# Kernel tuning notes

Hardware: AMD Instinct MI355X
Metric: run time of the kernel (lower is better)

The kernel has to match this reference:

```python
import jax, jax.numpy as jnp
import numpy as np

ANCHORS = np.array([[4.63,1.97,1.74],[6.93,2.51,2.84],[6.37,2.85,3.19],[10.5,2.94,3.47],
                    [12.29,2.9,3.87],[0.5,2.53,0.98],[2.11,0.77,1.47],[1.7,0.6,1.28],
                    [0.73,0.67,1.77],[0.41,0.41,1.07]], dtype=np.float32)  # [10,3] nuScenes anchor sizes
BINS = 20          # anchor_size_bins
TEXT_DIM = 3 * BINS
NUM_PROPOSALS = 200
NMS_K = 3


def _vector_values():
    la = np.log(ANCHORS)
    return np.linspace(la.min() - 0.1, la.max() - 0.1, BINS).astype(np.float32)


def _anchor_vecs_normed():
    # soft_relu_bin_vectors: soft-bin log-anchors into BINS bins per dim, dim-major flatten
    vals = _vector_values()
    inc = vals[1] - vals[0]
    la = np.log(ANCHORS)                                      # [10,3]
    v = np.clip((la[:, :, None] - vals[None, None, :]) / inc, 0.0, 1.0)  # [10,3,BINS]
    v = v.reshape(10, TEXT_DIM)
    return (v / (1e-8 + np.linalg.norm(v, axis=1, keepdims=True))).astype(np.float32)


def conv2d(x, w, b=None):
    y = jax.lax.conv_general_dilated(x, w, (1, 1), 'SAME',
                                     dimension_numbers=('NCHW', 'OIHW', 'NCHW'))
    if b is not None:
        y = y + b[None, :, None, None]
    return y


def iou_sim_vec(a):
    # vectorized form of the triple-nested loop: prod over dims of min/max ratio
    mn = jnp.minimum(a[:, None, :], a[None, :, :])
    mx = jnp.maximum(a[:, None, :], a[None, :, :])
    return jnp.prod(mn / mx, axis=-1)                         # [10,10]


def setup_inputs() -> dict:
    key = jax.random.key(0)
    ks = jax.random.split(key, 8)
    B, Cin, hid, H, W = 2, 512, 128, 180, 180
    feats = jax.random.normal(ks[0], (B, Cin, H, W), jnp.float32)
    w_shared = jax.random.normal(ks[1], (hid, Cin, 3, 3), jnp.float32) * 0.02
    b_shared = jnp.zeros((hid,), jnp.float32)
    w_bb = jax.random.normal(ks[2], (hid, hid, 3, 3), jnp.float32) * 0.05
    gamma_bb = jnp.ones((hid,), jnp.float32)
    beta_bb = jnp.zeros((hid,), jnp.float32)
    w_hm = jax.random.normal(ks[3], (TEXT_DIM, hid, 3, 3), jnp.float32) * 0.05
    b_hm = jnp.zeros((TEXT_DIM,), jnp.float32)
    thr_scale = jnp.ones((1,), jnp.float32)                   # Threshold2d scale
    logit_scale = jnp.ones((1,), jnp.float32) * np.log(1.0 / 0.07)
    logit_bias = jnp.ones((1,), jnp.float32) * (-10.0)
    w_enc = jax.random.normal(ks[4], (hid, 3), jnp.float32) * 0.1  # Conv1d(3->hid, k=1)
    anchor_vecs = jnp.asarray(_anchor_vecs_normed())
    xs = jnp.arange(W, dtype=jnp.float32) + 0.5
    ys = jnp.arange(H, dtype=jnp.float32) + 0.5
    gy, gx = jnp.meshgrid(ys, xs, indexing='ij')
    bev_pos = jnp.stack([gx.reshape(-1), gy.reshape(-1)], axis=-1)  # [H*W, 2]
    return dict(feats=feats, w_shared=w_shared, b_shared=b_shared, w_bb=w_bb,
                gamma_bb=gamma_bb, beta_bb=beta_bb, w_hm=w_hm, b_hm=b_hm,
                thr_scale=thr_scale, logit_scale=logit_scale, logit_bias=logit_bias,
                w_enc=w_enc, anchor_vecs=anchor_vecs, bev_pos=bev_pos)


def reference(feats, w_shared, b_shared, w_bb, gamma_bb, beta_bb, w_hm, b_hm,
              thr_scale, logit_scale, logit_bias, w_enc, anchor_vecs, bev_pos):
    B, _, H, W = feats.shape
    # shared conv
    lidar_feat = conv2d(feats, w_shared, b_shared)            # [B,hid,H,W]
    # BasicBlock2D: conv + (inference) BN + ReLU
    x = conv2d(lidar_feat, w_bb)
    x = jax.nn.relu(x * gamma_bb[None, :, None, None] + beta_bb[None, :, None, None])
    # heatmap conv -> Threshold2d (sigmoid((x - thresholds) * scale))
    vec = conv2d(x, w_hm, b_hm)                               # [B,60,H,W]
    thresholds = jnp.asarray(np.tile(_vector_values(), 3))[None, :, None, None]
    vec = jax.nn.sigmoid((vec - thresholds) * thr_scale[0])
    # cosine sim vs normalized anchor bin-vectors -> per-class heatmap
    vecn = vec / (1e-8 + jnp.linalg.norm(vec, axis=1, keepdims=True))
    sim = jnp.einsum('bchw,kc->bkhw', vecn, anchor_vecs)      # [B,10,H,W]
    heatmap = jax.nn.sigmoid(logit_scale[0] * sim + logit_bias[0])
    # NMS: keep only local maxima within nms_kernel_size window
    local_max = jax.lax.reduce_window(heatmap, -jnp.inf, jax.lax.max,
                                      (1, 1, NMS_K, NMS_K), (1, 1, 1, 1), 'SAME')
    hm_nms = jnp.where(heatmap == local_max, heatmap, 0.0)
    # top-k proposals over classes x positions
    flat = hm_nms.reshape(B, -1)                              # [B, 10*H*W]
    top_scores, top_idx = jax.lax.top_k(flat, NUM_PROPOSALS)
    top_labels = top_idx // (H * W)                           # [B,P]
    top_pos = top_idx % (H * W)                               # [B,P]
    # gather proposal features, heatmap scores and bev positions
    hid = lidar_feat.shape[1]
    lidar_flat = lidar_feat.reshape(B, hid, H * W)
    idx_f = jnp.broadcast_to(top_pos[:, None, :], (B, hid, NUM_PROPOSALS))
    query_feat = jnp.take_along_axis(lidar_flat, idx_f, axis=2)  # [B,hid,P]
    hm_flat = heatmap.reshape(B, 10, H * W)
    idx_h = jnp.broadcast_to(top_pos[:, None, :], (B, 10, NUM_PROPOSALS))
    query_hm_score = jnp.take_along_axis(hm_flat, idx_h, axis=2)  # [B,10,P]
    query_pos = bev_pos[top_pos]                              # [B,P,2]
    # anchor value encoding (Conv1d(3->hid,k=1) on log-anchor sizes of top classes)
    top_anchor = jnp.log(jnp.asarray(ANCHORS))[top_labels]    # [B,P,3]
    query_feat = query_feat + jnp.einsum('cd,bpd->bcp', w_enc, top_anchor)
    sims = iou_sim_vec(jnp.asarray(ANCHORS))                  # [10,10] anchor IoU similarity
    return heatmap, top_scores, top_labels, query_feat, query_pos, query_hm_score, sims
```

## Files before the change

### kernel.cpp

```cpp
#include <hip/hip_runtime.h>
#include <math.h>


#define HW 180
#define NPIX 32400
#define NCLS 10
#define NPROP 200
#define HID 128
#define TDIM 60
#define NBIG (NCLS*NPIX)

#define TH_LO  (-0.9915981193)
#define TH_STEP (0.1789675812)

__constant__ float c_anchors[10][3] = {
  {4.63f,1.97f,1.74f},{6.93f,2.51f,2.84f},{6.37f,2.85f,3.19f},{10.5f,2.94f,3.47f},
  {12.29f,2.9f,3.87f},{0.5f,2.53f,0.98f},{2.11f,0.77f,1.47f},{1.7f,0.6f,1.28f},
  {0.73f,0.67f,1.77f},{0.41f,0.41f,1.07f}};

using f16x8 = _Float16 __attribute__((ext_vector_type(8)));
using f16x4 = _Float16 __attribute__((ext_vector_type(4)));
using f32x4 = float    __attribute__((ext_vector_type(4)));

#define GLD_LDS16(g, l) __builtin_amdgcn_global_load_lds( \
    (__attribute__((address_space(1))) void*)(g), \
    (__attribute__((address_space(3))) void*)(l), 16, 0, 0)

template<int CIN, int KS, int HALVES>
__global__ void transpose_w_mfma(const float* __restrict__ w, _Float16* __restrict__ dst,
                                 int cout) {
  const int N = HALVES * KS * 36864;
  int i = blockIdx.x * 256 + threadIdx.x;
  if (i >= N) return;
  int j = i & 7;
  int lane = (i >> 3) & 63;
  int mf = (i >> 9) & 3;
  int rest = i >> 11;
  int tsl = rest % 9; rest /= 9;
  int t = (tsl % 3) * 3 + (tsl / 3);
  int plane = rest & 1; rest >>= 1;
  int ks = rest % KS; int h = rest / KS;
  int co = h * 64 + mf * 16 + (lane & 15);
  int ch = ks * 32 + (lane >> 4) * 8 + j;
  float v = (co < cout) ? w[((size_t)co * CIN + ch) * 9 + t] : 0.f;
  _Float16 hi = (_Float16)v;
  dst[i] = plane ? (_Float16)(v - (float)hi) : hi;
}

__global__ __launch_bounds__(256)
void convert_feats(const float* __restrict__ feats, _Float16* __restrict__ X1) {
  int px = blockIdx.x * 256 + threadIdx.x;
  int b = blockIdx.y >> 4, ks = blockIdx.y & 15;
  if (px >= NPIX) return;
  const float* src = feats + ((size_t)(b * 512 + ks * 32)) * NPIX + px;
  float v[32];
#pragma unroll
  for (int c = 0; c < 32; ++c) v[c] = src[(size_t)c * NPIX];
  f16x8 hv[4], lv[4];
#pragma unroll
  for (int c = 0; c < 32; ++c) {
    _Float16 h = (_Float16)v[c];
    hv[c >> 3][c & 7] = h;
    lv[c >> 3][c & 7] = (_Float16)(v[c] - (float)h);
  }
  size_t ob = ((size_t)(b * 16 + ks) * NPIX + px) * 32;
#pragma unroll
  for (int i = 0; i < 4; ++i) {
    *(f16x8*)(X1 + ob + i * 8) = hv[i];
    *(f16x8*)(X1 + 33177600u + ob + i * 8) = lv[i];
  }
}

template<int KS, int EPI>
__global__ __launch_bounds__(256, 2)
void conv_mfma(const _Float16* __restrict__ X, const _Float16* __restrict__ W,
               const float* __restrict__ p0, const float* __restrict__ p1,
               float* __restrict__ out0, _Float16* __restrict__ outX,
               const float* __restrict__ thr_scale, const float* __restrict__ logit_scale,
               const float* __restrict__ logit_bias, const float* __restrict__ anchor_vecs) {
  constexpr unsigned XPS = 2u * KS * NPIX * 32;
  extern __shared__ _Float16 dlds[];
  _Float16* lds_x = dlds;
  _Float16* lds_w = dlds + 25344;
  float* lds_av = (float*)(dlds + 37632);

  const int x0 = blockIdx.x * 16;
  const int y0 = blockIdx.y * 20;
  const int b  = (EPI == 2) ? blockIdx.z : (blockIdx.z >> 1);
  const int h  = (EPI == 2) ? 0 : (blockIdx.z & 1);
  const int tid = threadIdx.x;
  const int wave = tid >> 6;
  const int lane = tid & 63;
  const int xl = lane & 15, kg = lane >> 4;

  {
    unsigned* p = (unsigned*)lds_x;
    for (int i = tid; i < 12672; i += 256) p[i] = 0u;
    if (EPI == 2)
      for (int i = tid; i < 600; i += 256) lds_av[i] = anchor_vecs[i];
  }

  unsigned offs[13]; unsigned okb = 0;
#pragma unroll
  for (int s = 0; s < 13; ++s) {
    int inst = wave + 4 * s;
    int c = inst * 64 + lane;
    bool valid = (inst < 50) && (c < 3168);
    int plane = (c >= 1584) ? 1 : 0;
    int cc = c - plane * 1584;
    int px = cc >> 2, q = cc & 3;
    int r = px / 18, xx = px - r * 18;
    int gy = y0 - 1 + r, gx = x0 - 1 + xx;
    bool ok = valid && ((unsigned)gy < 180u) && ((unsigned)gx < 180u);
    offs[s] = ok ? ((unsigned)((b * KS) * NPIX + gy * 180 + gx) * 32u + (unsigned)q * 8u
                    + (unsigned)plane * XPS) : 0u;
    okb |= (ok ? 1u : 0u) << s;
  }

  f32x4 acc[4][5];
#pragma unroll
  for (int mf = 0; mf < 4; ++mf)
#pragma unroll
    for (int f = 0; f < 5; ++f) acc[mf][f] = (f32x4){0.f, 0.f, 0.f, 0.f};

  const _Float16* gwb = W + (size_t)(h * KS) * 36864;
  for (int ks = 0; ks < KS; ++ks) {
    const unsigned kof = (unsigned)ks * (NPIX * 32u);
    const _Float16* gw = gwb + (size_t)ks * 36864;
#pragma unroll
    for (int g = 0; g < 3; ++g) {
      __syncthreads();
      if (g == 0) {
#pragma unroll
        for (int s = 0; s < 13; ++s) {
          if (okb & (1u << s))
            GLD_LDS16(X + (size_t)(offs[s] + kof), lds_x + (wave + 4 * s) * 512);
        }
      }
#pragma unroll
      for (int s = 0; s < 6; ++s) {
        int c2 = wave + 4 * s;
        int pl = c2 / 12, idx = c2 - pl * 12;
        GLD_LDS16(gw + pl * 18432 + g * 6144 + idx * 512 + lane * 8,
                  lds_w + pl * 6144 + idx * 512);
      }
      __syncthreads();

      f16x8 bfh[7], bfl[7];
#pragma unroll
      for (int rr = 0; rr < 7; ++rr) {
        int lo = ((5 * wave + rr) * 18 + xl + g) * 32 + kg * 8;
        bfh[rr] = *(const f16x8*)(lds_x + lo);
        bfl[rr] = *(const f16x8*)(lds_x + 12672 + lo);
      }
#pragma unroll
      for (int ky = 0; ky < 3; ++ky) {
        const _Float16* wt = lds_w + ky * 2048 + lane * 8;
        f16x8 ah[4], al[4];
#pragma unroll
        for (int mf = 0; mf < 4; ++mf) {
          ah[mf] = *(const f16x8*)(wt + mf * 512);
          al[mf] = *(const f16x8*)(wt + 6144 + mf * 512);
        }
#pragma unroll
        for (int mf = 0; mf < 4; ++mf)
#pragma unroll
          for (int f = 0; f < 5; ++f) {
            acc[mf][f] = __builtin_amdgcn_mfma_f32_16x16x32_f16(ah[mf], bfh[f + ky], acc[mf][f], 0, 0, 0);
            acc[mf][f] = __builtin_amdgcn_mfma_f32_16x16x32_f16(ah[mf], bfl[f + ky], acc[mf][f], 0, 0, 0);
            acc[mf][f] = __builtin_amdgcn_mfma_f32_16x16x32_f16(al[mf], bfh[f + ky], acc[mf][f], 0, 0, 0);
          }
      }
    }
  }

  const int x = x0 + xl;
  if (EPI != 2) {
    if (x >= HW) return;
#pragma unroll
    for (int mf = 0; mf < 4; ++mf) {
      const int cobase = h * 64 + mf * 16 + kg * 4;
      f32x4 q0 = *(const f32x4*)(p0 + cobase);
      f32x4 q1 = (EPI == 1) ? *(const f32x4*)(p1 + cobase) : (f32x4){0.f,0.f,0.f,0.f};
#pragma unroll
      for (int f = 0; f < 5; ++f) {
        const int y = y0 + 5 * wave + f;
        const int kso = cobase >> 5, c32 = cobase & 31;
        size_t nidx = ((size_t)(b * 4 + kso) * NPIX + (size_t)y * 180 + x) * 32 + c32;
        if (EPI == 0) {
          f32x4 v;
          f16x4 h4, l4;
#pragma unroll
          for (int r = 0; r < 4; ++r) {
            float z = acc[mf][f][r] + q0[r];
            v[r] = z;
            _Float16 hh = (_Float16)z;
            h4[r] = hh;
            l4[r] = (_Float16)(z - (float)hh);
          }
          *(f32x4*)(out0 + nidx) = v;
          *(f16x4*)(outX + nidx) = h4;
          *(f16x4*)(outX + 8294400u + nidx) = l4;
        } else {
          f16x4 h4, l4;
#pragma unroll
          for (int r = 0; r < 4; ++r) {
            float z = fmaf(acc[mf][f][r], q0[r], q1[r]);
            z = fmaxf(z, 0.f);
            _Float16 hh = (_Float16)z;
            h4[r] = hh;
            l4[r] = (_Float16)(z - (float)hh);
          }
          *(f16x4*)(outX + nidx) = h4;
          *(f16x4*)(outX + 8294400u + nidx) = l4;
        }
      }
    }
  } else {
    const float s  = thr_scale[0];
    const float ls = logit_scale[0];
    const float lb = logit_bias[0];
    float bh4[4][4], th4[4][4];
    bool vmask[4];
#pragma unroll
    for (int mf = 0; mf < 4; ++mf) {
      const int cb = mf * 16 + kg * 4;
      vmask[mf] = (cb < TDIM);
#pragma unroll
      for (int r = 0; r < 4; ++r) {
        bh4[mf][r] = vmask[mf] ? p0[cb + r] : 0.f;
        th4[mf][r] = (float)(TH_LO + (double)((cb + r) % 20) * TH_STEP);
      }
    }
#pragma unroll
    for (int f = 0; f < 5; ++f) {
      const int y = y0 + 5 * wave + f;
      float v[4][4];
      float s2 = 0.f;
#pragma unroll
      for (int mf = 0; mf < 4; ++mf)
#pragma unroll
        for (int r = 0; r < 4; ++r) {
          float z = acc[mf][f][r] + bh4[mf][r];
          float t = (z - th4[mf][r]) * s;
          float vv = vmask[mf] ? 1.f / (1.f + expf(-t)) : 0.f;
          v[mf][r] = vv;
          s2 = fmaf(vv, vv, s2);
        }
      s2 += __shfl_xor(s2, 16);
      s2 += __shfl_xor(s2, 32);
      const float rs = 1.f / (1e-8f + sqrtf(s2));
      float hm[10];
#pragma unroll
      for (int k = 0; k < 10; ++k) {
        float d = 0.f;
#pragma unroll
        for (int mf = 0; mf < 4; ++mf) {
          const int cb = mf * 16 + kg * 4;
          f32x4 a = vmask[mf] ? *(const f32x4*)(lds_av + k * TDIM + cb)
                              : (f32x4){0.f, 0.f, 0.f, 0.f};
#pragma unroll
          for (int r = 0; r < 4; ++r) d = fmaf(v[mf][r], a[r], d);
        }
        d += __shfl_xor(d, 16);
        d += __shfl_xor(d, 32);
        hm[k] = 1.f / (1.f + expf(-fmaf(ls, d * rs, lb)));
      }
      if (y < HW && x < HW) {
#pragma unroll
        for (int j = 0; j < 3; ++j) {
          int k = kg + 4 * j;
          if (k < NCLS)
            out0[((size_t)(b * NCLS + k) * HW + y) * HW + x] = hm[k];
        }
      }
    }
  }
}

__global__ void sims_kernel(float* __restrict__ out_sims) {
  int t = threadIdx.x;
  if (t < 100) {
    int i = t / 10, j = t % 10;
    float r = 1.f;
#pragma unroll
    for (int d = 0; d < 3; ++d) {
      float ai = c_anchors[i][d], aj = c_anchors[j][d];
      r *= fminf(ai, aj) / fmaxf(ai, aj);
    }
    out_sims[t] = r;
  }
}

__global__ __launch_bounds__(256)
void nms_kernel(const float* __restrict__ hm, float* __restrict__ ckey,
                int* __restrict__ cidx, int* __restrict__ cnt) {
  __shared__ int lcnt[2];
  __shared__ int lbase[2];
  const int tid = threadIdx.x;
  if (tid < 2) lcnt[tid] = 0;
  __syncthreads();

  int i = blockIdx.x * 256 + tid;
  bool surv = false; float v = 0.f; int bk = 0, p = 0;
  if (i < 2 * NBIG) {
    int x = i % HW; int y = (i / HW) % HW; int plane = i / NPIX;
    v = hm[i];
    float m = v;
#pragma unroll
    for (int dy = -1; dy <= 1; ++dy)
#pragma unroll
      for (int dx = -1; dx <= 1; ++dx) {
        int yy = y + dy, xx = x + dx;
        if ((unsigned)yy < (unsigned)HW && (unsigned)xx < (unsigned)HW)
          m = fmaxf(m, hm[((size_t)plane * NPIX) + yy * HW + xx]);
      }
    if (v == m) {
      surv = true;
      bk = i / NBIG;
      p = atomicAdd(&lcnt[bk], 1);
    }
  }
  __syncthreads();
  if (tid < 2 && lcnt[tid] > 0)
    lbase[tid] = atomicAdd(&cnt[tid], lcnt[tid]);
  __syncthreads();
  if (surv) {
    int slot = lbase[bk] + p;
    ckey[(size_t)bk * NBIG + slot] = v;
    cidx[(size_t)bk * NBIG + slot] = i - bk * NBIG;
  }
}

__global__ __launch_bounds__(1024)
void topk_kernel(const float* __restrict__ ckey, const int* __restrict__ cidx,
                 const int* __restrict__ cnt, const float* __restrict__ heatmap,
                 const float* __restrict__ bev_pos, float* __restrict__ out,
                 int* __restrict__ iws) {
  const int b = blockIdx.x;
  const int tid = threadIdx.x;
  const float* keys = ckey + (size_t)b * NBIG;
  const int* idxs = cidx + (size_t)b * NBIG;

  __shared__ unsigned hist[256];
  __shared__ unsigned sh_prefix;
  __shared__ int sh_want, sh_n;
  __shared__ int cntGT, cntTie;
  __shared__ unsigned gt_key[256], gt_idx[256];
  __shared__ unsigned tie_idx[2048];

  if (tid == 0) sh_n = cnt[b];
  __syncthreads();
  const int n = sh_n;

  unsigned prefix = 0; int want = NPROP;
  for (int shift = 24; shift >= 0; shift -= 8) {
    if (tid < 256) hist[tid] = 0u;
    __syncthreads();
    for (int i = tid; i < n; i += 1024) {
      unsigned k = __float_as_uint(keys[i]);
      bool match = (shift == 24) || ((k >> (shift + 8)) == (prefix >> (shift + 8)));
      if (match) atomicAdd(&hist[(k >> shift) & 255], 1u);
    }
    __syncthreads();
    if (tid == 0) {
      int cum = 0; int bsel = 0; sh_want = want;
      for (int bin = 255; bin >= 0; --bin) {
        cum += (int)hist[bin];
        if (cum >= want) { bsel = bin; sh_want = want - (cum - (int)hist[bin]); break; }
      }
      sh_prefix = prefix | ((unsigned)bsel << shift);
      cntGT = 0; cntTie = 0;
    }
    __syncthreads();
    prefix = sh_prefix; want = sh_want;
    __syncthreads();
  }
  const unsigned T = prefix;

  for (int i = tid; i < n; i += 1024) {
    unsigned k = __float_as_uint(keys[i]);
    if (k > T) {
      int p = atomicAdd(&cntGT, 1);
      if (p < 256) { gt_key[p] = k; gt_idx[p] = (unsigned)idxs[i]; }
    } else if (k == T) {
      int p = atomicAdd(&cntTie, 1);
      if (p < 2048) tie_idx[p] = (unsigned)idxs[i];
    }
  }
  __syncthreads();
  const int nGT = min(cntGT, 256);
  const int nTie = min(cntTie, 2048);

  for (int i = tid; i < 256; i += 1024)
    if (i >= nGT) { gt_key[i] = 0u; gt_idx[i] = 0xFFFFFFFFu; }
  for (int i = tid; i < 2048; i += 1024)
    if (i >= nTie) tie_idx[i] = 0xFFFFFFFFu;
  __syncthreads();

  for (int k2 = 2; k2 <= 256; k2 <<= 1) {
    for (int j = k2 >> 1; j > 0; j >>= 1) {
      for (int i = tid; i < 256; i += 1024) {
        int ixj = i ^ j;
        if (ixj > i) {
          unsigned ka = gt_key[i], kb = gt_key[ixj];
          unsigned ia = gt_idx[i], ib = gt_idx[ixj];
          bool firstA = (ka > kb) || (ka == kb && ia < ib);
          bool up = ((i & k2) == 0);
          if (up ? !firstA : firstA) {
            gt_key[i] = kb; gt_key[ixj] = ka;
            gt_idx[i] = ib; gt_idx[ixj] = ia;
          }
        }
      }
      __syncthreads();
    }
  }
  for (int k2 = 2; k2 <= 2048; k2 <<= 1) {
    for (int j = k2 >> 1; j > 0; j >>= 1) {
      for (int i = tid; i < 2048; i += 1024) {
        int ixj = i ^ j;
        if (ixj > i) {
          unsigned ia = tie_idx[i], ib = tie_idx[ixj];
          bool firstA = ia < ib;
          bool up = ((i & k2) == 0);
          if (up ? !firstA : firstA) { tie_idx[i] = ib; tie_idx[ixj] = ia; }
        }
      }
      __syncthreads();
    }
  }

  for (int r = tid; r < NPROP; r += 1024) {
    unsigned idx; float score;
    if (r < nGT) { idx = gt_idx[r]; score = __uint_as_float(gt_key[r]); }
    else         { idx = tie_idx[r - nGT]; score = __uint_as_float(T); }
    int label = (int)(idx / NPIX);
    int pos = (int)(idx - (unsigned)label * NPIX);
    out[648000 + b * NPROP + r] = score;
    out[648400 + b * NPROP + r] = (float)label;
    out[700000 + (b * NPROP + r) * 2 + 0] = bev_pos[pos * 2 + 0];
    out[700000 + (b * NPROP + r) * 2 + 1] = bev_pos[pos * 2 + 1];
#pragma unroll
    for (int k = 0; k < NCLS; ++k)
      out[700800 + (b * NCLS + k) * NPROP + r] = heatmap[(size_t)(b * NCLS + k) * NPIX + pos];
    iws[b * NPROP + r] = pos;
    iws[2 * NPROP + b * NPROP + r] = label;
  }
}

__global__ void gather_qf_kernel(const float* __restrict__ lidar, const float* __restrict__ w_enc,
                                 const int* __restrict__ iws, float* __restrict__ out_qf) {
  int p = blockIdx.x % NPROP;
  int b = blockIdx.x / NPROP;
  int c = threadIdx.x;
  int pos = iws[b * NPROP + p];
  int label = iws[2 * NPROP + b * NPROP + p];
  float la0 = logf(c_anchors[label][0]);
  float la1 = logf(c_anchors[label][1]);
  float la2 = logf(c_anchors[label][2]);
  float dot = w_enc[c * 3 + 0] * la0 + w_enc[c * 3 + 1] * la1 + w_enc[c * 3 + 2] * la2;
  float g = lidar[((size_t)(b * 4 + (c >> 5)) * NPIX + pos) * 32 + (c & 31)];
  out_qf[((size_t)b * HID + c) * NPROP + p] = g + dot;
}

extern "C" void kernel_launch(void* const* d_in, const int* in_sizes, int n_in,
                              void* d_out, int out_size, void* d_ws, size_t ws_size,
                              hipStream_t stream) {
  (void)in_sizes; (void)n_in; (void)out_size; (void)ws_size;
  const float* feats       = (const float*)d_in[0];
  const float* w_shared    = (const float*)d_in[1];
  const float* b_shared    = (const float*)d_in[2];
  const float* w_bb        = (const float*)d_in[3];
  const float* gamma_bb    = (const float*)d_in[4];
  const float* beta_bb     = (const float*)d_in[5];
  const float* w_hm        = (const float*)d_in[6];
  const float* b_hm        = (const float*)d_in[7];
  const float* thr_scale   = (const float*)d_in[8];
  const float* logit_scale = (const float*)d_in[9];
  const float* logit_bias  = (const float*)d_in[10];
  const float* w_enc       = (const float*)d_in[11];
  const float* anchor_vecs = (const float*)d_in[12];
  const float* bev_pos     = (const float*)d_in[13];
  float* out = (float*)d_out;

  float* ws = (float*)d_ws;
  size_t off = 0;
  _Float16* X1 = (_Float16*)(ws + off); off += 33177600;
  _Float16* X2 = (_Float16*)(ws + off); off += 8294400;
  float* lidarN = ws + off; off += 8294400;
  _Float16* X3 = (_Float16*)(ws + off); off += 8294400;
  _Float16* W1 = (_Float16*)(ws + off); off += 589824;
  _Float16* W2 = (_Float16*)(ws + off); off += 147456;
  _Float16* W3 = (_Float16*)(ws + off); off += 73728;
  float* ckey  = ws + off; off += (size_t)2 * NBIG;
  int*   cidx  = (int*)(ws + off); off += (size_t)2 * NBIG;
  int*   iws   = (int*)(ws + off); off += 800;
  int*   cnt   = (int*)(ws + off);

  transpose_w_mfma<512,16,2><<<(2*16*36864 + 255)/256, 256, 0, stream>>>(w_shared, W1, 128);
  transpose_w_mfma<128, 4,2><<<(2*4*36864  + 255)/256, 256, 0, stream>>>(w_bb, W2, 128);
  transpose_w_mfma<128, 4,1><<<(1*4*36864  + 255)/256, 256, 0, stream>>>(w_hm, W3, 60);
  convert_feats<<<dim3(127, 32), 256, 0, stream>>>(feats, X1);

  const unsigned CONV_LDS = (25344 + 12288) * sizeof(_Float16);
  const unsigned HEAD_LDS = CONV_LDS + 600 * sizeof(float);
  dim3 cgrid(12, 9, 4);
  conv_mfma<16,0><<<cgrid, 256, CONV_LDS, stream>>>(X1, W1, b_shared, nullptr, lidarN, X2,
                                                    nullptr, nullptr, nullptr, nullptr);
  conv_mfma<4, 1><<<cgrid, 256, CONV_LDS, stream>>>(X2, W2, gamma_bb, beta_bb, nullptr, X3,
                                                    nullptr, nullptr, nullptr, nullptr);
  dim3 hgrid(12, 9, 2);
  conv_mfma<4, 2><<<hgrid, 256, HEAD_LDS, stream>>>(X3, W3, b_hm, nullptr, out, nullptr,
                                                    thr_scale, logit_scale, logit_bias,
                                                    anchor_vecs);

  sims_kernel<<<1, 128, 0, stream>>>(out + 704800);
  hipMemsetAsync(cnt, 0, 2 * sizeof(int), stream);
  nms_kernel<<<(2*NBIG + 255)/256, 256, 0, stream>>>(out, ckey, cidx, cnt);
  topk_kernel<<<2, 1024, 0, stream>>>(ckey, cidx, cnt, out, bev_pos, out, iws);
  gather_qf_kernel<<<2*NPROP, 128, 0, stream>>>(lidarN, w_enc, iws, out + 648800);
}
```

Baseline: 539.0 us.

## Shrink conv row tile, double-buffer weight loads, and merge prep kernels

Each conv block now covers 12 rows instead of 20, which gives a 12x15 grid and smaller LDS and accumulator footprints. The two non-head convs keep two LDS weight buffers so the next weight slice is loaded while the current one is computed. The weight transposes, feature conversion, anchor-similarity computation and counter reset are merged into one prep kernel to cut launch overhead. In exchange the halo overhead per output row rises and LDS per block goes up for the double-buffered variants, which may limit occupancy.

```diff
diff --git a/kernel.cpp b/kernel.cpp
--- a/kernel.cpp
+++ b/kernel.cpp
@@ -26,11 +26,9 @@
     (__attribute__((address_space(1))) void*)(g), \
     (__attribute__((address_space(3))) void*)(l), 16, 0, 0)
 
-template<int CIN, int KS, int HALVES>
-__global__ void transpose_w_mfma(const float* __restrict__ w, _Float16* __restrict__ dst,
-                                 int cout) {
-  const int N = HALVES * KS * 36864;
-  int i = blockIdx.x * 256 + threadIdx.x;
+__device__ __forceinline__ void w_tr(const float* __restrict__ w, _Float16* __restrict__ dst,
+                                     int CIN, int KS, int HALVES, int cout, int i) {
+  int N = HALVES * KS * 36864;
   if (i >= N) return;
   int j = i & 7;
   int lane = (i >> 3) & 63;
@@ -48,27 +46,53 @@
 }
 
 __global__ __launch_bounds__(256)
-void convert_feats(const float* __restrict__ feats, _Float16* __restrict__ X1) {
-  int px = blockIdx.x * 256 + threadIdx.x;
-  int b = blockIdx.y >> 4, ks = blockIdx.y & 15;
-  if (px >= NPIX) return;
-  const float* src = feats + ((size_t)(b * 512 + ks * 32)) * NPIX + px;
-  float v[32];
-#pragma unroll
-  for (int c = 0; c < 32; ++c) v[c] = src[(size_t)c * NPIX];
-  f16x8 hv[4], lv[4];
-#pragma unroll
-  for (int c = 0; c < 32; ++c) {
-    _Float16 h = (_Float16)v[c];
-    hv[c >> 3][c & 7] = h;
-    lv[c >> 3][c & 7] = (_Float16)(v[c] - (float)h);
-  }
-  size_t ob = ((size_t)(b * 16 + ks) * NPIX + px) * 32;
-#pragma unroll
-  for (int i = 0; i < 4; ++i) {
-    *(f16x8*)(X1 + ob + i * 8) = hv[i];
-    *(f16x8*)(X1 + 33177600u + ob + i * 8) = lv[i];
-  }
+void prep_kernel(const float* __restrict__ w_shared, const float* __restrict__ w_bb,
+                 const float* __restrict__ w_hm, const float* __restrict__ feats,
+                 _Float16* __restrict__ W1, _Float16* __restrict__ W2,
+                 _Float16* __restrict__ W3, _Float16* __restrict__ X1,
+                 float* __restrict__ out_sims, int* __restrict__ cnt) {
+  int bid = blockIdx.x;
+  const int tid = threadIdx.x;
+  if (bid < 4608) { w_tr(w_shared, W1, 512, 16, 2, 128, bid * 256 + tid); return; }
+  bid -= 4608;
+  if (bid < 1152) { w_tr(w_bb, W2, 128, 4, 2, 128, bid * 256 + tid); return; }
+  bid -= 1152;
+  if (bid < 576)  { w_tr(w_hm, W3, 128, 4, 1, 60, bid * 256 + tid); return; }
+  bid -= 576;
+  if (bid < 4064) {
+    int px = (bid % 127) * 256 + tid;
+    int bks = bid / 127; int b = bks >> 4; int ks = bks & 15;
+    if (px >= NPIX) return;
+    const float* src = feats + ((size_t)(b * 512 + ks * 32)) * NPIX + px;
+    float v[32];
+#pragma unroll
+    for (int c = 0; c < 32; ++c) v[c] = src[(size_t)c * NPIX];
+    f16x8 hv[4], lv[4];
+#pragma unroll
+    for (int c = 0; c < 32; ++c) {
+      _Float16 h = (_Float16)v[c];
+      hv[c >> 3][c & 7] = h;
+      lv[c >> 3][c & 7] = (_Float16)(v[c] - (float)h);
+    }
+    size_t ob = ((size_t)(b * 16 + ks) * NPIX + px) * 32;
+#pragma unroll
+    for (int i = 0; i < 4; ++i) {
+      *(f16x8*)(X1 + ob + i * 8) = hv[i];
+      *(f16x8*)(X1 + 33177600u + ob + i * 8) = lv[i];
+    }
+    return;
+  }
+  if (tid < 100) {
+    int i = tid / 10, j = tid % 10;
+    float r = 1.f;
+#pragma unroll
+    for (int d = 0; d < 3; ++d) {
+      float ai = c_anchors[i][d], aj = c_anchors[j][d];
+      r *= fminf(ai, aj) / fmaxf(ai, aj);
+    }
+    out_sims[tid] = r;
+  }
+  if (tid == 128) { cnt[0] = 0; cnt[1] = 0; }
 }
 
 template<int KS, int EPI>
@@ -79,13 +103,15 @@
                const float* __restrict__ thr_scale, const float* __restrict__ logit_scale,
                const float* __restrict__ logit_bias, const float* __restrict__ anchor_vecs) {
   constexpr unsigned XPS = 2u * KS * NPIX * 32;
+  constexpr bool DBUF = (EPI != 2);
   extern __shared__ _Float16 dlds[];
   _Float16* lds_x = dlds;
-  _Float16* lds_w = dlds + 25344;
-  float* lds_av = (float*)(dlds + 37632);
+  _Float16* wA = dlds + 16128;
+  _Float16* wB = dlds + 28416;
+  float* lds_av = (float*)(dlds + 28416);
 
   const int x0 = blockIdx.x * 16;
-  const int y0 = blockIdx.y * 20;
+  const int y0 = blockIdx.y * 12;
   const int b  = (EPI == 2) ? blockIdx.z : (blockIdx.z >> 1);
   const int h  = (EPI == 2) ? 0 : (blockIdx.z & 1);
   const int tid = threadIdx.x;
@@ -95,19 +121,19 @@
 
   {
     unsigned* p = (unsigned*)lds_x;
-    for (int i = tid; i < 12672; i += 256) p[i] = 0u;
+    for (int i = tid; i < 8064; i += 256) p[i] = 0u;
     if (EPI == 2)
       for (int i = tid; i < 600; i += 256) lds_av[i] = anchor_vecs[i];
   }
 
-  unsigned offs[13]; unsigned okb = 0;
-#pragma unroll
-  for (int s = 0; s < 13; ++s) {
+  unsigned offs[8]; unsigned okb = 0;
+#pragma unroll
+  for (int s = 0; s < 8; ++s) {
     int inst = wave + 4 * s;
     int c = inst * 64 + lane;
-    bool valid = (inst < 50) && (c < 3168);
-    int plane = (c >= 1584) ? 1 : 0;
-    int cc = c - plane * 1584;
+    bool valid = (c < 2016);
+    int plane = (c >= 1008) ? 1 : 0;
+    int cc = c - plane * 1008;
     int px = cc >> 2, q = cc & 3;
     int r = px / 18, xx = px - r * 18;
     int gy = y0 - 1 + r, gx = x0 - 1 + xx;
@@ -117,59 +143,80 @@
     okb |= (ok ? 1u : 0u) << s;
   }
 
-  f32x4 acc[4][5];
+  f32x4 acc[4][3];
 #pragma unroll
   for (int mf = 0; mf < 4; ++mf)
 #pragma unroll
-    for (int f = 0; f < 5; ++f) acc[mf][f] = (f32x4){0.f, 0.f, 0.f, 0.f};
+    for (int f = 0; f < 3; ++f) acc[mf][f] = (f32x4){0.f, 0.f, 0.f, 0.f};
+
+  auto COMPUTE = [&](int g, const _Float16* wbuf) {
+    f16x8 bfh[5], bfl[5];
+#pragma unroll
+    for (int rr = 0; rr < 5; ++rr) {
+      int lo = ((3 * wave + rr) * 18 + xl + g) * 32 + kg * 8;
+      bfh[rr] = *(const f16x8*)(lds_x + lo);
+      bfl[rr] = *(const f16x8*)(lds_x + 8064 + lo);
+    }
+#pragma unroll
+    for (int ky = 0; ky < 3; ++ky) {
+      const _Float16* wt = wbuf + ky * 2048 + lane * 8;
+      f16x8 ah[4], al[4];
+#pragma unroll
+      for (int mf = 0; mf < 4; ++mf) {
+        ah[mf] = *(const f16x8*)(wt + mf * 512);
+        al[mf] = *(const f16x8*)(wt + 6144 + mf * 512);
+      }
+#pragma unroll
+      for (int mf = 0; mf < 4; ++mf)
+#pragma unroll
+        for (int f = 0; f < 3; ++f) {
+          acc[mf][f] = __builtin_amdgcn_mfma_f32_16x16x32_f16(ah[mf], bfh[f + ky], acc[mf][f], 0, 0, 0);
+          acc[mf][f] = __builtin_amdgcn_mfma_f32_16x16x32_f16(ah[mf], bfl[f + ky], acc[mf][f], 0, 0, 0);
+          acc[mf][f] = __builtin_amdgcn_mfma_f32_16x16x32_f16(al[mf], bfh[f + ky], acc[mf][f], 0, 0, 0);
+        }
+    }
+  };
+  auto WDMA = [&](const _Float16* gw, int g, _Float16* wbuf) {
+#pragma unroll
+    for (int s = 0; s < 6; ++s) {
+      int c2 = wave + 4 * s;
+      int pl = c2 / 12, idx = c2 - pl * 12;
+      GLD_LDS16(gw + pl * 18432 + g * 6144 + idx * 512 + lane * 8,
+                wbuf + pl * 6144 + idx * 512);
+    }
+  };
+  auto XDMA = [&](unsigned kof) {
+#pragma unroll
+    for (int s = 0; s < 8; ++s) {
+      if (okb & (1u << s))
+        GLD_LDS16(X + (size_t)(offs[s] + kof), lds_x + (wave + 4 * s) * 512);
+    }
+  };
 
   const _Float16* gwb = W + (size_t)(h * KS) * 36864;
   for (int ks = 0; ks < KS; ++ks) {
     const unsigned kof = (unsigned)ks * (NPIX * 32u);
     const _Float16* gw = gwb + (size_t)ks * 36864;
-#pragma unroll
-    for (int g = 0; g < 3; ++g) {
+    if (DBUF) {
       __syncthreads();
-      if (g == 0) {
-#pragma unroll
-        for (int s = 0; s < 13; ++s) {
-          if (okb & (1u << s))
-            GLD_LDS16(X + (size_t)(offs[s] + kof), lds_x + (wave + 4 * s) * 512);
-        }
-      }
-#pragma unroll
-      for (int s = 0; s < 6; ++s) {
-        int c2 = wave + 4 * s;
-        int pl = c2 / 12, idx = c2 - pl * 12;
-        GLD_LDS16(gw + pl * 18432 + g * 6144 + idx * 512 + lane * 8,
-                  lds_w + pl * 6144 + idx * 512);
-      }
+      XDMA(kof);
+      WDMA(gw, 0, wA);
       __syncthreads();
-
-      f16x8 bfh[7], bfl[7];
-#pragma unroll
-      for (int rr = 0; rr < 7; ++rr) {
-        int lo = ((5 * wave + rr) * 18 + xl + g) * 32 + kg * 8;
-        bfh[rr] = *(const f16x8*)(lds_x + lo);
-        bfl[rr] = *(const f16x8*)(lds_x + 12672 + lo);
-      }
-#pragma unroll
-      for (int ky = 0; ky < 3; ++ky) {
-        const _Float16* wt = lds_w + ky * 2048 + lane * 8;
-        f16x8 ah[4], al[4];
-#pragma unroll
-        for (int mf = 0; mf < 4; ++mf) {
-          ah[mf] = *(const f16x8*)(wt + mf * 512);
-          al[mf] = *(const f16x8*)(wt + 6144 + mf * 512);
-        }
-#pragma unroll
-        for (int mf = 0; mf < 4; ++mf)
-#pragma unroll
-          for (int f = 0; f < 5; ++f) {
-            acc[mf][f] = __builtin_amdgcn_mfma_f32_16x16x32_f16(ah[mf], bfh[f + ky], acc[mf][f], 0, 0, 0);
-            acc[mf][f] = __builtin_amdgcn_mfma_f32_16x16x32_f16(ah[mf], bfl[f + ky], acc[mf][f], 0, 0, 0);
-            acc[mf][f] = __builtin_amdgcn_mfma_f32_16x16x32_f16(al[mf], bfh[f + ky], acc[mf][f], 0, 0, 0);
-          }
+      WDMA(gw, 1, wB);
+      COMPUTE(0, wA);
+      __syncthreads();
+      WDMA(gw, 2, wA);
+      COMPUTE(1, wB);
+      __syncthreads();
+      COMPUTE(2, wA);
+    } else {
+#pragma unroll
+      for (int g = 0; g < 3; ++g) {
+        __syncthreads();
+        if (g == 0) XDMA(kof);
+        WDMA(gw, g, wA);
+        __syncthreads();
+        COMPUTE(g, wA);
       }
     }
   }
@@ -183,8 +230,8 @@
       f32x4 q0 = *(const f32x4*)(p0 + cobase);
       f32x4 q1 = (EPI == 1) ? *(const f32x4*)(p1 + cobase) : (f32x4){0.f,0.f,0.f,0.f};
 #pragma unroll
-      for (int f = 0; f < 5; ++f) {
-        const int y = y0 + 5 * wave + f;
+      for (int f = 0; f < 3; ++f) {
+        const int y = y0 + 3 * wave + f;
         const int kso = cobase >> 5, c32 = cobase & 31;
         size_t nidx = ((size_t)(b * 4 + kso) * NPIX + (size_t)y * 180 + x) * 32 + c32;
         if (EPI == 0) {
@@ -233,8 +280,8 @@
       }
     }
 #pragma unroll
-    for (int f = 0; f < 5; ++f) {
-      const int y = y0 + 5 * wave + f;
+    for (int f = 0; f < 3; ++f) {
+      const int y = y0 + 3 * wave + f;
       float v[4][4];
       float s2 = 0.f;
 #pragma unroll
@@ -266,7 +313,7 @@
         d += __shfl_xor(d, 32);
         hm[k] = 1.f / (1.f + expf(-fmaf(ls, d * rs, lb)));
       }
-      if (y < HW && x < HW) {
+      if (x < HW) {
 #pragma unroll
         for (int j = 0; j < 3; ++j) {
           int k = kg + 4 * j;
@@ -275,20 +322,6 @@
         }
       }
     }
-  }
-}
-
-__global__ void sims_kernel(float* __restrict__ out_sims) {
-  int t = threadIdx.x;
-  if (t < 100) {
-    int i = t / 10, j = t % 10;
-    float r = 1.f;
-#pragma unroll
-    for (int d = 0; d < 3; ++d) {
-      float ai = c_anchors[i][d], aj = c_anchors[j][d];
-      r *= fminf(ai, aj) / fmaxf(ai, aj);
-    }
-    out_sims[t] = r;
   }
 }
 
@@ -498,25 +531,21 @@
   int*   iws   = (int*)(ws + off); off += 800;
   int*   cnt   = (int*)(ws + off);
 
-  transpose_w_mfma<512,16,2><<<(2*16*36864 + 255)/256, 256, 0, stream>>>(w_shared, W1, 128);
-  transpose_w_mfma<128, 4,2><<<(2*4*36864  + 255)/256, 256, 0, stream>>>(w_bb, W2, 128);
-  transpose_w_mfma<128, 4,1><<<(1*4*36864  + 255)/256, 256, 0, stream>>>(w_hm, W3, 60);
-  convert_feats<<<dim3(127, 32), 256, 0, stream>>>(feats, X1);
-
-  const unsigned CONV_LDS = (25344 + 12288) * sizeof(_Float16);
-  const unsigned HEAD_LDS = CONV_LDS + 600 * sizeof(float);
-  dim3 cgrid(12, 9, 4);
+  prep_kernel<<<10401, 256, 0, stream>>>(w_shared, w_bb, w_hm, feats,
+                                         W1, W2, W3, X1, out + 704800, cnt);
+
+  const unsigned CONV_LDS = 81408;
+  const unsigned HEAD_LDS = 59232;
+  dim3 cgrid(12, 15, 4);
   conv_mfma<16,0><<<cgrid, 256, CONV_LDS, stream>>>(X1, W1, b_shared, nullptr, lidarN, X2,
                                                     nullptr, nullptr, nullptr, nullptr);
   conv_mfma<4, 1><<<cgrid, 256, CONV_LDS, stream>>>(X2, W2, gamma_bb, beta_bb, nullptr, X3,
                                                     nullptr, nullptr, nullptr, nullptr);
-  dim3 hgrid(12, 9, 2);
+  dim3 hgrid(12, 15, 2);
   conv_mfma<4, 2><<<hgrid, 256, HEAD_LDS, stream>>>(X3, W3, b_hm, nullptr, out, nullptr,
                                                     thr_scale, logit_scale, logit_bias,
                                                     anchor_vecs);
 
-  sims_kernel<<<1, 128, 0, stream>>>(out + 704800);
-  hipMemsetAsync(cnt, 0, 2 * sizeof(int), stream);
   nms_kernel<<<(2*NBIG + 255)/256, 256, 0, stream>>>(out, ckey, cidx, cnt);
   topk_kernel<<<2, 1024, 0, stream>>>(ckey, cidx, cnt, out, bev_pos, out, iws);
   gather_qf_kernel<<<2*NPROP, 128, 0, stream>>>(lidarN, w_enc, iws, out + 648800);
```

Result: faster. 519.8 us (-3.6%).
